# Performance work log

Hardware: AMD Instinct MI355X
Metric: run time of the kernel (lower is better)

Reference implementation:

```python
import jax, jax.numpy as jnp
from jax import lax
import numpy as np

KH, KW = 9, 9  # box-filter window (kernel=(9,9))
IN_CH = 1


def _box_sum(x):
    # F.conv2d(x, ones([1, in_ch, KH, KW]), stride=1, padding=(4, 4))
    k = jnp.ones((1, IN_CH, KH, KW), x.dtype)
    pad = ((KH - 1) // 2, (KH - 1) // 2), ((KW - 1) // 2, (KW - 1) // 2)
    return lax.conv_general_dilated(
        x, k, window_strides=(1, 1), padding=pad,
        dimension_numbers=("NCHW", "OIHW", "NCHW"))


def setup_inputs() -> dict:
    key = jax.random.key(0)
    k1, k2 = jax.random.split(key)
    B, C, H, W = 32, IN_CH, 512, 512
    inp = jax.random.normal(k1, (B, C, H, W), dtype=jnp.float32)
    tgt = jax.random.uniform(k2, (B, C, H, W), dtype=jnp.float32)
    return {"input": inp, "target": tgt}


def reference(input, target):
    # normalize target from [-1, 1] -> [0, 1]
    t = (target + 1.0) * 0.5
    II = input * input
    TT = t * t
    IT = input * t

    T_sum = _box_sum(t)
    I_sum = _box_sum(input)
    TT_sum = _box_sum(TT)
    II_sum = _box_sum(II)
    IT_sum = _box_sum(IT)

    ksize = float(KH * KW)
    Ihat = I_sum / ksize
    That = T_sum / ksize

    cross = IT_sum - Ihat * T_sum - That * I_sum + That * Ihat * ksize
    T_var = TT_sum - 2.0 * That * T_sum + That * That * ksize
    I_var = II_sum - 2.0 * Ihat * I_sum + Ihat * Ihat * ksize

    cc = cross * cross / (T_var * I_var + 1e-5)
    return -1.0 * jnp.mean(cc)
```

## Files before the change

kernel.cpp:

```cpp
#include <hip/hip_runtime.h>

#define IMG_H 512
#define IMG_W 512
#define N_IMG 32
#define ROWS  8
#define BANDS (IMG_H / ROWS)
#define ITERS (ROWS + 8)
#define WROW  520
#define NPIX  (32.0f * 512.0f * 512.0f)

__device__ __forceinline__ void load8(const float* __restrict__ ip,
                                      const float* __restrict__ tp,
                                      int r, int c0, float* I, float* T) {
    if (r >= 0 && r < IMG_H) {
        const float* irow = ip + (ptrdiff_t)r * IMG_W + c0;
        const float* trow = tp + (ptrdiff_t)r * IMG_W + c0;
        float4 a = *(const float4*)(irow);
        float4 b = *(const float4*)(irow + 4);
        float4 c = *(const float4*)(trow);
        float4 d = *(const float4*)(trow + 4);
        I[0]=a.x; I[1]=a.y; I[2]=a.z; I[3]=a.w;
        I[4]=b.x; I[5]=b.y; I[6]=b.z; I[7]=b.w;
        T[0]=fmaf(c.x,0.5f,0.5f); T[1]=fmaf(c.y,0.5f,0.5f);
        T[2]=fmaf(c.z,0.5f,0.5f); T[3]=fmaf(c.w,0.5f,0.5f);
        T[4]=fmaf(d.x,0.5f,0.5f); T[5]=fmaf(d.y,0.5f,0.5f);
        T[6]=fmaf(d.z,0.5f,0.5f); T[7]=fmaf(d.w,0.5f,0.5f);
    } else {
        #pragma unroll
        for (int j = 0; j < 8; ++j) { I[j] = 0.0f; T[j] = 0.0f; }
    }
}

__device__ __forceinline__ void hsum8(const float4 L, const float* o, const float4 R,
                                      float* h) {
    float s = ((L.x + L.y) + (L.z + L.w)) + ((o[0] + o[1]) + (o[2] + o[3])) + o[4];
    h[0] = s;
    s += o[5] - L.x;  h[1] = s;
    s += o[6] - L.y;  h[2] = s;
    s += o[7] - L.z;  h[3] = s;
    s += R.x  - L.w;  h[4] = s;
    s += R.y  - o[0]; h[5] = s;
    s += R.z  - o[1]; h[6] = s;
    s += R.w  - o[2]; h[7] = s;
}

__device__ __forceinline__ float cc_of(float sI, float sT, float sII, float sTT, float sIT) {
    const float inv81 = 1.0f / 81.0f;
    float u     = sI * inv81;
    float w     = sT * inv81;
    float cross = fmaf(-u, sT, sIT);
    float iv    = fmaf(-u, sI, sII);
    float tv    = fmaf(-w, sT, sTT);
    float den   = fmaf(tv, iv, 1e-5f);
    return cross * cross * __builtin_amdgcn_rcpf(den);
}

__global__ __launch_bounds__(256)
void cc_loss_kernel(const float* __restrict__ in, const float* __restrict__ tg,
                    float* __restrict__ out) {
    __shared__ __align__(16) float lds[4][5][WROW];
    __shared__ float red[4];

    const int t    = threadIdx.x;
    const int w    = t >> 6;
    const int lane = t & 63;

    const int gband = blockIdx.x * 4 + w;
    const int b     = gband >> 6;
    const int band  = gband & 63;
    const int r0    = band * ROWS;
    const size_t base = (size_t)b * (IMG_H * IMG_W);
    const float* ip = in + base;
    const float* tp = tg + base;
    const int c0    = lane * 8;

    float* ldsw = &lds[w][0][0];

    if (lane < 8) {
        const int pos = (lane & 3) + ((lane & 4) ? 516 : 0);
        #pragma unroll
        for (int a = 0; a < 5; ++a) ldsw[a * WROW + pos] = 0.0f;
    }
    __builtin_amdgcn_wave_barrier();

    float vI[8] = {}, vT[8] = {}, vII[8] = {}, vTT[8] = {}, vIT[8] = {};
    float acc = 0.0f;

    float pLI[8], pLT[8], pQI[8], pQT[8];
    float nLI[8], nLT[8], nQI[8], nQT[8];

    load8(ip, tp, r0 - 4, c0, pLI, pLT);
    #pragma unroll
    for (int j = 0; j < 8; ++j) { pQI[j] = 0.0f; pQT[j] = 0.0f; }

    for (int it = 0; it < ITERS; ++it) {
        if (it + 1 < ITERS) {
            load8(ip, tp, r0 - 3 + it, c0, nLI, nLT);
            const int tr = r0 + it - 12;
            load8(ip, tp, (it >= 8) ? tr : -1, c0, nQI, nQT);
        }

        #pragma unroll
        for (int j = 0; j < 8; ++j) {
            float dI = pLI[j] - pQI[j], aI = pLI[j] + pQI[j];
            float dT = pLT[j] - pQT[j], aT = pLT[j] + pQT[j];
            vI[j]  += dI;
            vT[j]  += dT;
            vII[j]  = fmaf(dI, aI, vII[j]);
            vTT[j]  = fmaf(dT, aT, vTT[j]);
            float m = pQI[j] * pQT[j];
            vIT[j]  = fmaf(pLI[j], pLT[j], vIT[j] - m);
        }

        if (it >= 8) {
            float* p0 = ldsw + 0 * WROW + 4 + c0;
            float* p1 = ldsw + 1 * WROW + 4 + c0;
            float* p2 = ldsw + 2 * WROW + 4 + c0;
            float* p3 = ldsw + 3 * WROW + 4 + c0;
            float* p4 = ldsw + 4 * WROW + 4 + c0;
            ((float4*)p0)[0] = make_float4(vI[0],  vI[1],  vI[2],  vI[3]);
            ((float4*)p0)[1] = make_float4(vI[4],  vI[5],  vI[6],  vI[7]);
            ((float4*)p1)[0] = make_float4(vT[0],  vT[1],  vT[2],  vT[3]);
            ((float4*)p1)[1] = make_float4(vT[4],  vT[5],  vT[6],  vT[7]);
            ((float4*)p2)[0] = make_float4(vII[0], vII[1], vII[2], vII[3]);
            ((float4*)p2)[1] = make_float4(vII[4], vII[5], vII[6], vII[7]);
            ((float4*)p3)[0] = make_float4(vTT[0], vTT[1], vTT[2], vTT[3]);
            ((float4*)p3)[1] = make_float4(vTT[4], vTT[5], vTT[6], vTT[7]);
            ((float4*)p4)[0] = make_float4(vIT[0], vIT[1], vIT[2], vIT[3]);
            ((float4*)p4)[1] = make_float4(vIT[4], vIT[5], vIT[6], vIT[7]);
            __builtin_amdgcn_wave_barrier();

            float4 L0 = *(const float4*)(ldsw + 0 * WROW + c0);
            float4 R0 = *(const float4*)(ldsw + 0 * WROW + 12 + c0);
            float4 L1 = *(const float4*)(ldsw + 1 * WROW + c0);
            float4 R1 = *(const float4*)(ldsw + 1 * WROW + 12 + c0);
            float4 L2 = *(const float4*)(ldsw + 2 * WROW + c0);
            float4 R2 = *(const float4*)(ldsw + 2 * WROW + 12 + c0);
            float4 L3 = *(const float4*)(ldsw + 3 * WROW + c0);
            float4 R3 = *(const float4*)(ldsw + 3 * WROW + 12 + c0);
            float4 L4 = *(const float4*)(ldsw + 4 * WROW + c0);
            float4 R4 = *(const float4*)(ldsw + 4 * WROW + 12 + c0);

            float h0[8], h1[8], h2[8], h3[8], h4[8];
            hsum8(L0, vI,  R0, h0);
            hsum8(L1, vT,  R1, h1);
            hsum8(L2, vII, R2, h2);
            hsum8(L3, vTT, R3, h3);
            hsum8(L4, vIT, R4, h4);
            #pragma unroll
            for (int j = 0; j < 8; ++j)
                acc += cc_of(h0[j], h1[j], h2[j], h3[j], h4[j]);
            __builtin_amdgcn_wave_barrier();
        }

        #pragma unroll
        for (int j = 0; j < 8; ++j) {
            pLI[j] = nLI[j]; pLT[j] = nLT[j];
            pQI[j] = nQI[j]; pQT[j] = nQT[j];
        }
    }

    #pragma unroll
    for (int off = 32; off > 0; off >>= 1) acc += __shfl_down(acc, off);
    if (lane == 0) red[w] = acc;
    __syncthreads();
    if (t == 0)
        atomicAdd(out, (red[0] + red[1] + red[2] + red[3]) * (-1.0f / NPIX));
}

extern "C" void kernel_launch(void* const* d_in, const int* in_sizes, int n_in,
                              void* d_out, int out_size, void* d_ws, size_t ws_size,
                              hipStream_t stream) {
    const float* in = (const float*)d_in[0];
    const float* tg = (const float*)d_in[1];
    float* out = (float*)d_out;

    hipMemsetAsync(out, 0, sizeof(float), stream);
    dim3 grid(N_IMG * BANDS / 4);
    cc_loss_kernel<<<grid, 256, 0, stream>>>(in, tg, out);
}
```

Before: 111.9 us.

## Replace LDS horizontal halo exchange with wave shuffles and halve rows per band

The horizontal 9-tap sum no longer stages the column sums in shared memory. It now pulls the neighbouring lanes' four halo values with __shfl_up/__shfl_down, which drops the LDS stores, loads and wave barriers. Rows per wave band also drop from 8 to 4, doubling the grid for more parallelism. The cost is that the 8-row vertical warm-up is repeated over fewer output rows, so redundant global loads and arithmetic grow substantially.

```diff
diff --git a/kernel.cpp b/kernel.cpp
--- a/kernel.cpp
+++ b/kernel.cpp
@@ -3,10 +3,9 @@
 #define IMG_H 512
 #define IMG_W 512
 #define N_IMG 32
-#define ROWS  8
+#define ROWS  4
 #define BANDS (IMG_H / ROWS)
 #define ITERS (ROWS + 8)
-#define WROW  520
 #define NPIX  (32.0f * 512.0f * 512.0f)
 
 __device__ __forceinline__ void load8(const float* __restrict__ ip,
@@ -31,17 +30,29 @@
     }
 }
 
-__device__ __forceinline__ void hsum8(const float4 L, const float* o, const float4 R,
-                                      float* h) {
-    float s = ((L.x + L.y) + (L.z + L.w)) + ((o[0] + o[1]) + (o[2] + o[3])) + o[4];
+__device__ __forceinline__ void hsum8_shfl(const float* o, float* h, bool nf, bool nl) {
+    float Lx = __shfl_up(o[4], 1, 64);
+    float Ly = __shfl_up(o[5], 1, 64);
+    float Lz = __shfl_up(o[6], 1, 64);
+    float Lw = __shfl_up(o[7], 1, 64);
+    float Rx = __shfl_down(o[0], 1, 64);
+    float Ry = __shfl_down(o[1], 1, 64);
+    float Rz = __shfl_down(o[2], 1, 64);
+    float Rw = __shfl_down(o[3], 1, 64);
+    Lx = nf ? Lx : 0.0f;  Ly = nf ? Ly : 0.0f;
+    Lz = nf ? Lz : 0.0f;  Lw = nf ? Lw : 0.0f;
+    Rx = nl ? Rx : 0.0f;  Ry = nl ? Ry : 0.0f;
+    Rz = nl ? Rz : 0.0f;  Rw = nl ? Rw : 0.0f;
+
+    float s = ((Lx + Ly) + (Lz + Lw)) + ((o[0] + o[1]) + (o[2] + o[3])) + o[4];
     h[0] = s;
-    s += o[5] - L.x;  h[1] = s;
-    s += o[6] - L.y;  h[2] = s;
-    s += o[7] - L.z;  h[3] = s;
-    s += R.x  - L.w;  h[4] = s;
-    s += R.y  - o[0]; h[5] = s;
-    s += R.z  - o[1]; h[6] = s;
-    s += R.w  - o[2]; h[7] = s;
+    s += o[5] - Lx;  h[1] = s;
+    s += o[6] - Ly;  h[2] = s;
+    s += o[7] - Lz;  h[3] = s;
+    s += Rx   - Lw;  h[4] = s;
+    s += Ry   - o[0]; h[5] = s;
+    s += Rz   - o[1]; h[6] = s;
+    s += Rw   - o[2]; h[7] = s;
 }
 
 __device__ __forceinline__ float cc_of(float sI, float sT, float sII, float sTT, float sIT) {
@@ -58,7 +69,6 @@
 __global__ __launch_bounds__(256)
 void cc_loss_kernel(const float* __restrict__ in, const float* __restrict__ tg,
                     float* __restrict__ out) {
-    __shared__ __align__(16) float lds[4][5][WROW];
     __shared__ float red[4];
 
     const int t    = threadIdx.x;
@@ -66,22 +76,15 @@
     const int lane = t & 63;
 
     const int gband = blockIdx.x * 4 + w;
-    const int b     = gband >> 6;
-    const int band  = gband & 63;
+    const int b     = gband >> 7;
+    const int band  = gband & (BANDS - 1);
     const int r0    = band * ROWS;
     const size_t base = (size_t)b * (IMG_H * IMG_W);
     const float* ip = in + base;
     const float* tp = tg + base;
     const int c0    = lane * 8;
-
-    float* ldsw = &lds[w][0][0];
-
-    if (lane < 8) {
-        const int pos = (lane & 3) + ((lane & 4) ? 516 : 0);
-        #pragma unroll
-        for (int a = 0; a < 5; ++a) ldsw[a * WROW + pos] = 0.0f;
-    }
-    __builtin_amdgcn_wave_barrier();
+    const bool nf   = (lane != 0);
+    const bool nl   = (lane != 63);
 
     float vI[8] = {}, vT[8] = {}, vII[8] = {}, vTT[8] = {}, vIT[8] = {};
     float acc = 0.0f;
@@ -113,44 +116,15 @@
         }
 
         if (it >= 8) {
-            float* p0 = ldsw + 0 * WROW + 4 + c0;
-            float* p1 = ldsw + 1 * WROW + 4 + c0;
-            float* p2 = ldsw + 2 * WROW + 4 + c0;
-            float* p3 = ldsw + 3 * WROW + 4 + c0;
-            float* p4 = ldsw + 4 * WROW + 4 + c0;
-            ((float4*)p0)[0] = make_float4(vI[0],  vI[1],  vI[2],  vI[3]);
-            ((float4*)p0)[1] = make_float4(vI[4],  vI[5],  vI[6],  vI[7]);
-            ((float4*)p1)[0] = make_float4(vT[0],  vT[1],  vT[2],  vT[3]);
-            ((float4*)p1)[1] = make_float4(vT[4],  vT[5],  vT[6],  vT[7]);
-            ((float4*)p2)[0] = make_float4(vII[0], vII[1], vII[2], vII[3]);
-            ((float4*)p2)[1] = make_float4(vII[4], vII[5], vII[6], vII[7]);
-            ((float4*)p3)[0] = make_float4(vTT[0], vTT[1], vTT[2], vTT[3]);
-            ((float4*)p3)[1] = make_float4(vTT[4], vTT[5], vTT[6], vTT[7]);
-            ((float4*)p4)[0] = make_float4(vIT[0], vIT[1], vIT[2], vIT[3]);
-            ((float4*)p4)[1] = make_float4(vIT[4], vIT[5], vIT[6], vIT[7]);
-            __builtin_amdgcn_wave_barrier();
-
-            float4 L0 = *(const float4*)(ldsw + 0 * WROW + c0);
-            float4 R0 = *(const float4*)(ldsw + 0 * WROW + 12 + c0);
-            float4 L1 = *(const float4*)(ldsw + 1 * WROW + c0);
-            float4 R1 = *(const float4*)(ldsw + 1 * WROW + 12 + c0);
-            float4 L2 = *(const float4*)(ldsw + 2 * WROW + c0);
-            float4 R2 = *(const float4*)(ldsw + 2 * WROW + 12 + c0);
-            float4 L3 = *(const float4*)(ldsw + 3 * WROW + c0);
-            float4 R3 = *(const float4*)(ldsw + 3 * WROW + 12 + c0);
-            float4 L4 = *(const float4*)(ldsw + 4 * WROW + c0);
-            float4 R4 = *(const float4*)(ldsw + 4 * WROW + 12 + c0);
-
             float h0[8], h1[8], h2[8], h3[8], h4[8];
-            hsum8(L0, vI,  R0, h0);
-            hsum8(L1, vT,  R1, h1);
-            hsum8(L2, vII, R2, h2);
-            hsum8(L3, vTT, R3, h3);
-            hsum8(L4, vIT, R4, h4);
+            hsum8_shfl(vI,  h0, nf, nl);
+            hsum8_shfl(vT,  h1, nf, nl);
+            hsum8_shfl(vII, h2, nf, nl);
+            hsum8_shfl(vTT, h3, nf, nl);
+            hsum8_shfl(vIT, h4, nf, nl);
             #pragma unroll
             for (int j = 0; j < 8; ++j)
                 acc += cc_of(h0[j], h1[j], h2[j], h3[j], h4[j]);
-            __builtin_amdgcn_wave_barrier();
         }
 
         #pragma unroll
@@ -161,7 +135,7 @@
     }
 
     #pragma unroll
-    for (int off = 32; off > 0; off >>= 1) acc += __shfl_down(acc, off);
+    for (int off = 32; off > 0; off >>= 1) acc += __shfl_down(acc, off, 64);
     if (lane == 0) red[w] = acc;
     __syncthreads();
     if (t == 0)
```

Result: slower. 121.8 us (+8.8%).
